# Kernel tuning notes

Measured on AMD Instinct MI355X. Metric: run time of the kernel, lower is better.

Reference implementation:

```python
import jax, jax.numpy as jnp
import numpy as np

B, N, D, E, H = 8, 2048, 1024, 8, 4096
CAP_FACTOR = 1.25   # capacity_factor_train
THRESHOLD = 0.2     # second_threshold_train
LOSS_COEF = 0.01
MIN_CAP = 4
EPS = 1e-9


def setup_inputs() -> dict:
    key = jax.random.key(0)
    ks = jax.random.split(key, 5)
    return {
        "hidden_states": jax.random.normal(ks[0], (B, N, D), jnp.float32),
        "wg": jax.random.normal(ks[1], (D, E), jnp.float32) * 0.02,
        "w1": jax.random.normal(ks[2], (E, D, H), jnp.float32) * 0.02,
        "b1": jnp.zeros((E, H), jnp.float32),
        "w2": jax.random.normal(ks[3], (E, H, D), jnp.float32) * 0.02,
        "b2": jnp.zeros((E, D), jnp.float32),
        "rand_probs": jax.random.uniform(ks[4], (B, N), jnp.float32),
    }


def _top2_gating(x, wg, rand_probs):
    # GShard-style top-2 gating with 'random' second policy and capacity limit.
    dt = x.dtype
    n = x.shape[-2]
    e = wg.shape[-1]
    raw = jax.nn.softmax(jnp.einsum('bnd,de->bne', x, wg), axis=-1)  # [b,n,e]
    idx1 = jnp.argmax(raw, axis=-1)
    gate1 = jnp.max(raw, axis=-1)
    mask1 = jax.nn.one_hot(idx1, e, dtype=dt)
    raw2 = raw * (1.0 - mask1)
    idx2 = jnp.argmax(raw2, axis=-1)
    gate2 = jnp.max(raw2, axis=-1)
    mask2 = jax.nn.one_hot(idx2, e, dtype=dt)
    denom = gate1 + gate2 + EPS
    gate1 = gate1 / denom
    gate2 = gate2 / denom
    # load-balancing loss (computed before capacity truncation)
    density1 = jnp.mean(mask1, axis=-2)          # [b,e]
    density1_proxy = jnp.mean(raw, axis=-2)      # [b,e]
    loss = jnp.mean(density1_proxy * density1) * (e * e)
    # second policy == 'random': keep 2nd expert w.p. ~ gate2/threshold
    mask2 = mask2 * (rand_probs < (gate2 / max(THRESHOLD, EPS)))[..., None].astype(dt)
    capacity = max(min(n, int(n * CAP_FACTOR / e)), MIN_CAP)
    # exclusive cumsum over tokens -> position within expert
    pos1 = (jnp.cumsum(mask1, axis=-2) - mask1) * mask1
    mask1 = mask1 * (pos1 < capacity).astype(dt)
    mask1_count = jnp.sum(mask1, axis=-2, keepdims=True)
    mask1_flat = jnp.sum(mask1, axis=-1)
    pos1 = jnp.sum(pos1, axis=-1)
    gate1 = gate1 * mask1_flat
    pos2 = (jnp.cumsum(mask2, axis=-2) - mask2 + mask1_count) * mask2
    mask2 = mask2 * (pos2 < capacity).astype(dt)
    mask2_flat = jnp.sum(mask2, axis=-1)
    pos2 = jnp.sum(pos2, axis=-1)
    gate2 = gate2 * mask2_flat
    # combine tensor [b,n,e,c]; out-of-range positions one_hot to zeros
    oh_p1 = jax.nn.one_hot(pos1.astype(jnp.int32), capacity, dtype=dt)
    oh_p2 = jax.nn.one_hot(pos2.astype(jnp.int32), capacity, dtype=dt)
    combine = ((gate1 * mask1_flat)[..., None, None]
               * jax.nn.one_hot(idx1, e, dtype=dt)[..., None] * oh_p1[..., None, :]
               + (gate2 * mask2_flat)[..., None, None]
               * jax.nn.one_hot(idx2, e, dtype=dt)[..., None] * oh_p2[..., None, :])
    dispatch = (combine > 0).astype(dt)
    return dispatch, combine, loss


def reference(hidden_states, wg, w1, b1, w2, b2, rand_probs):
    dispatch, combine, loss = _top2_gating(hidden_states, wg, rand_probs)
    # dispatch tokens to per-expert capacity buffers: [e,b,c,d]
    ei = jnp.einsum('bnd,bnec->ebcd', hidden_states, dispatch)
    # per-expert FFN (grouped GEMMs)
    h = jax.nn.gelu(jnp.einsum('ebcd,edh->ebch', ei, w1) + b1[:, None, None, :],
                    approximate=False)
    eo = jnp.einsum('ebch,ehd->ebcd', h, w2) + b2[:, None, None, :]
    # combine back to token order with gate weights
    out = jnp.einsum('ebcd,bnec->bnd', eo, combine)
    # dropout is identity (output_dropout_prob=0.0 / eval mode)
    return out, loss * LOSS_COEF
```

## Files before the change

kernel.cpp:

```cpp
#include <hip/hip_runtime.h>
#include <hip/hip_bf16.h>
#include <math.h>

#define BB 8
#define NN 2048
#define DD 1024
#define EE 8
#define HH 4096
#define CAP 320
#define NTOK (BB*NN)
#define MBC (BB*CAP)

typedef __bf16 bf16x8 __attribute__((ext_vector_type(8)));
typedef float f32x4 __attribute__((ext_vector_type(4)));
typedef unsigned u32x4 __attribute__((ext_vector_type(4)));
typedef unsigned short u16x4 __attribute__((ext_vector_type(4)));
typedef unsigned short u16;

__device__ __forceinline__ u16 f2bf(float f) {
    unsigned u = __builtin_bit_cast(unsigned, f);
    u += 0x7FFFu + ((u >> 16) & 1u);
    return (u16)(u >> 16);
}

__device__ __forceinline__ void async_cp16(const void* g, void* l) {
    __builtin_amdgcn_global_load_lds((const __attribute__((address_space(1))) void*)g,
                                     (__attribute__((address_space(3))) void*)l,
                                     16, 0, 0);
}

__global__ void MoE_zero_stats(float* stats) {
    if (threadIdx.x < 128) stats[threadIdx.x] = 0.0f;
}

__global__ __launch_bounds__(256) void MoE_gating(
    const float* __restrict__ x, const float* __restrict__ wg,
    const float* __restrict__ rp,
    int* __restrict__ i1o, int* __restrict__ i2o,
    float* __restrict__ g1o, float* __restrict__ g2o, int* __restrict__ keepo,
    float* __restrict__ proxy, float* __restrict__ cnt1)
{
    __shared__ float wgT[8*1024];
    __shared__ float sprox[8];
    __shared__ float scnt[8];
    int tid = threadIdx.x;
    {
        int d0 = tid*4;
        #pragma unroll
        for (int j = 0; j < 4; j++) {
            int d = d0 + j;
            f32x4 a = *(const f32x4*)(wg + d*8);
            f32x4 b = *(const f32x4*)(wg + d*8 + 4);
            wgT[0*1024+d]=a[0]; wgT[1*1024+d]=a[1]; wgT[2*1024+d]=a[2]; wgT[3*1024+d]=a[3];
            wgT[4*1024+d]=b[0]; wgT[5*1024+d]=b[1]; wgT[6*1024+d]=b[2]; wgT[7*1024+d]=b[3];
        }
    }
    if (tid < 8) { sprox[tid] = 0.0f; scnt[tid] = 0.0f; }
    __syncthreads();

    int wid = tid >> 6, lane = tid & 63;
    int tok = blockIdx.x*4 + wid;
    int b = tok >> 11;
    const float* xr = x + (size_t)tok * DD;

    double acc[8];
    #pragma unroll
    for (int e = 0; e < 8; e++) acc[e] = 0.0;
    for (int i = 0; i < 16; i++) {
        float xv = xr[i*64 + lane];
        #pragma unroll
        for (int e = 0; e < 8; e++)
            acc[e] += (double)xv * (double)wgT[e*1024 + i*64 + lane];
    }
    #pragma unroll
    for (int e = 0; e < 8; e++) {
        double v = acc[e];
        for (int off = 32; off; off >>= 1) v += __shfl_down(v, off, 64);
        acc[e] = v;
    }
    if (lane == 0) {
        float l[8];
        #pragma unroll
        for (int e = 0; e < 8; e++) l[e] = (float)acc[e];
        int i1 = 0;
        #pragma unroll
        for (int e = 1; e < 8; e++) if (l[e] > l[i1]) i1 = e;
        int i2 = (i1 == 0) ? 1 : 0;
        #pragma unroll
        for (int e = 0; e < 8; e++) if (e != i1 && l[e] > l[i2]) i2 = e;
        float mx = l[i1], p[8], s = 0.0f;
        #pragma unroll
        for (int e = 0; e < 8; e++) { p[e] = expf(l[e] - mx); s += p[e]; }
        float inv = 1.0f / s;
        #pragma unroll
        for (int e = 0; e < 8; e++) p[e] *= inv;
        float gate1 = p[i1], gate2 = p[i2];
        float denom = gate1 + gate2 + 1e-9f;
        float g1 = gate1 / denom, g2 = gate2 / denom;
        int keep = (rp[tok] < g2 / 0.2f) ? 1 : 0;
        i1o[tok] = i1; i2o[tok] = i2; g1o[tok] = g1; g2o[tok] = g2; keepo[tok] = keep;
        #pragma unroll
        for (int e = 0; e < 8; e++) atomicAdd(&sprox[e], p[e]);
        atomicAdd(&scnt[i1], 1.0f);
    }
    __syncthreads();
    if (tid < 8) {
        atomicAdd(&proxy[b*8 + tid], sprox[tid]);
        atomicAdd(&cnt1[b*8 + tid], scnt[tid]);
    }
}

__global__ __launch_bounds__(256) void MoE_scan(
    const int* __restrict__ i1, const int* __restrict__ i2, const int* __restrict__ keep,
    const float* __restrict__ g1, const float* __restrict__ g2,
    int* __restrict__ p1o, int* __restrict__ p2o,
    float* __restrict__ g1f, float* __restrict__ g2f,
    int* __restrict__ slot_token)
{
    int b = blockIdx.x, t = threadIdx.x;
    __shared__ unsigned long long s0[256], s1[256];
    for (int s = t; s < EE*CAP; s += 256) {
        int e = s / CAP, c = s % CAP;
        slot_token[(e*BB + b)*CAP + c] = -1;
    }
    int base = b*NN + t*8;

    int e1v[8];
    unsigned long long u0 = 0, u1 = 0;
    #pragma unroll
    for (int j = 0; j < 8; j++) {
        int e = i1[base + j]; e1v[j] = e;
        if (e < 4) u0 += 1ull << (e*16); else u1 += 1ull << ((e-4)*16);
    }
    s0[t] = u0; s1[t] = u1;
    __syncthreads();
    for (int off = 1; off < 256; off <<= 1) {
        unsigned long long a0 = 0, a1 = 0;
        if (t >= off) { a0 = s0[t-off]; a1 = s1[t-off]; }
        __syncthreads();
        s0[t] += a0; s1[t] += a1;
        __syncthreads();
    }
    unsigned long long t0 = s0[255], t1 = s1[255];
    unsigned long long x0 = s0[t] - u0, x1 = s1[t] - u1;
    int run[8], mc[8];
    #pragma unroll
    for (int e = 0; e < 8; e++) {
        run[e] = (int)((e < 4 ? (x0 >> (e*16)) : (x1 >> ((e-4)*16))) & 0xFFFF);
        int tot = (int)((e < 4 ? (t0 >> (e*16)) : (t1 >> ((e-4)*16))) & 0xFFFF);
        mc[e] = tot < CAP ? tot : CAP;
    }
    #pragma unroll
    for (int j = 0; j < 8; j++) {
        int e = e1v[j];
        int p = run[e]++;
        bool v = p < CAP;
        p1o[base + j] = p;
        g1f[base + j] = v ? g1[base + j] : 0.0f;
        if (v) slot_token[(e*BB + b)*CAP + p] = t*8 + j;
    }
    __syncthreads();

    int e2v[8], kv[8];
    u0 = 0; u1 = 0;
    #pragma unroll
    for (int j = 0; j < 8; j++) {
        int e = i2[base + j]; e2v[j] = e;
        int k = keep[base + j]; kv[j] = k;
        if (k) { if (e < 4) u0 += 1ull << (e*16); else u1 += 1ull << ((e-4)*16); }
    }
    s0[t] = u0; s1[t] = u1;
    __syncthreads();
    for (int off = 1; off < 256; off <<= 1) {
        unsigned long long a0 = 0, a1 = 0;
        if (t >= off) { a0 = s0[t-off]; a1 = s1[t-off]; }
        __syncthreads();
        s0[t] += a0; s1[t] += a1;
        __syncthreads();
    }
    x0 = s0[t] - u0; x1 = s1[t] - u1;
    #pragma unroll
    for (int e = 0; e < 8; e++)
        run[e] = mc[e] + (int)((e < 4 ? (x0 >> (e*16)) : (x1 >> ((e-4)*16))) & 0xFFFF);
    #pragma unroll
    for (int j = 0; j < 8; j++) {
        if (kv[j]) {
            int e = e2v[j];
            int p = run[e]++;
            bool v = p < CAP;
            p2o[base + j] = p;
            g2f[base + j] = v ? g2[base + j] : 0.0f;
            if (v) slot_token[(e*BB + b)*CAP + p] = t*8 + j;
        } else {
            p2o[base + j] = 0;
            g2f[base + j] = 0.0f;
        }
    }
}

__global__ __launch_bounds__(256) void MoE_dispatch(
    const float* __restrict__ x, const int* __restrict__ slot_token,
    u16* __restrict__ Abuf)
{
    int tid = threadIdx.x, wid = tid >> 6, lane = tid & 63;
    int slot = blockIdx.x*4 + wid;
    int b = (slot % (BB*CAP)) / CAP;
    int tok = slot_token[slot];
    u16* dst = Abuf + (size_t)slot * DD;
    if (tok >= 0) {
        const float* src = x + ((size_t)b*NN + tok) * DD;
        #pragma unroll
        for (int i = 0; i < 4; i++) {
            f32x4 v = *(const f32x4*)(src + (lane + 64*i)*4);
            u16x4 w = { f2bf(v[0]), f2bf(v[1]), f2bf(v[2]), f2bf(v[3]) };
            *(u16x4*)(dst + (lane + 64*i)*4) = w;
        }
    } else {
        u16x4 z = {0,0,0,0};
        #pragma unroll
        for (int i = 0; i < 4; i++) *(u16x4*)(dst + (lane + 64*i)*4) = z;
    }
}

__global__ __launch_bounds__(256) void MoE_transpose_bf16(
    const float* __restrict__ in, u16* __restrict__ out,
    int R, int C, int rTiles, int cTiles)
{
    int tilesPerE = rTiles * cTiles;
    int e = blockIdx.x / tilesPerE;
    int t = blockIdx.x % tilesPerE;
    int r0 = (t / cTiles) * 64, c0 = (t % cTiles) * 64;
    const float* ip = in + (size_t)e * R * C;
    u16* op = out + (size_t)e * R * C;
    __shared__ float T[64*65];
    int tid = threadIdx.x;
    int rr = tid >> 4, cx = tid & 15;
    #pragma unroll
    for (int i = 0; i < 4; i++) {
        int r = rr + i*16;
        f32x4 v = *(const f32x4*)(ip + (size_t)(r0 + r)*C + c0 + cx*4);
        float* d = T + r*65 + cx*4;
        d[0]=v[0]; d[1]=v[1]; d[2]=v[2]; d[3]=v[3];
    }
    __syncthreads();
    #pragma unroll
    for (int i = 0; i < 4; i++) {
        int c = rr + i*16;
        int r = cx*4;
        u16x4 w = { f2bf(T[(r+0)*65 + c]), f2bf(T[(r+1)*65 + c]),
                    f2bf(T[(r+2)*65 + c]), f2bf(T[(r+3)*65 + c]) };
        *(u16x4*)(op + (size_t)(c0 + c)*R + r0 + r) = w;
    }
}

template <int MODE>
__global__ __launch_bounds__(256, 2) void MoE_gemm_bt(
    const u16* __restrict__ Aall, const u16* __restrict__ Ball,
    void* __restrict__ Call, const float* __restrict__ biasAll,
    int M, int N, int K, int mTiles, int nTiles)
{
    int bid = blockIdx.x;
    int e = bid & 7;
    int i = bid >> 3;
    const int GM = 8;
    int group = i / (GM*nTiles);
    int gm = mTiles - group*GM; if (gm > GM) gm = GM;
    int rem = i - group*GM*nTiles;
    int n_ = rem / gm;
    int mm = rem % gm;
    if (n_ & 1) mm = gm - 1 - mm;
    int m0 = (group*GM + mm) * 128;
    int n0 = n_ * 128;

    const u16* A  = Aall + (size_t)e * M * K;
    const u16* Bm = Ball + (size_t)e * N * K;
    const float* bias = biasAll + (size_t)e * N;

    __shared__ u16 sA[128*32];
    __shared__ u16 sB[128*32];

    int tid = threadIdx.x;
    int lane = tid & 63, wid = tid >> 6;
    int wm = wid & 1, wn = wid >> 1;
    int l16 = lane & 15, quad = lane >> 4;

    int ch0 = tid, ch1 = 256 + tid;
    int r0c = ch0 >> 2, c0c = (ch0 & 3) ^ (r0c & 3);
    int r1c = ch1 >> 2, c1c = (ch1 & 3) ^ (r1c & 3);
    const u16* gA0 = A  + (size_t)(m0 + r0c)*K + c0c*8;
    const u16* gA1 = A  + (size_t)(m0 + r1c)*K + c1c*8;
    const u16* gB0 = Bm + (size_t)(n0 + r0c)*K + c0c*8;
    const u16* gB1 = Bm + (size_t)(n0 + r1c)*K + c1c*8;
    u16* dA0 = sA + (size_t)(tid & ~63) * 8;
    u16* dA1 = sA + (size_t)(256 + (tid & ~63)) * 8;
    u16* dB0 = sB + (size_t)(tid & ~63) * 8;
    u16* dB1 = sB + (size_t)(256 + (tid & ~63)) * 8;

    const u16* rA = sA + (wm*64 + l16)*32 + ((quad ^ (l16 & 3)) * 8);
    const u16* rB = sB + (wn*64 + l16)*32 + ((quad ^ (l16 & 3)) * 8);

    f32x4 acc[4][4] = {};
    int ksteps = K / 32;
    for (int kk = 0; kk < ksteps; ++kk) {
        async_cp16(gA0, dA0); async_cp16(gA1, dA1);
        async_cp16(gB0, dB0); async_cp16(gB1, dB1);
        gA0 += 32; gA1 += 32; gB0 += 32; gB1 += 32;
        __syncthreads();
        bf16x8 av[4], bv[4];
        #pragma unroll
        for (int i2 = 0; i2 < 4; i2++) av[i2] = __builtin_bit_cast(bf16x8, *(const u32x4*)(rA + i2*512));
        #pragma unroll
        for (int j = 0; j < 4; j++) bv[j] = __builtin_bit_cast(bf16x8, *(const u32x4*)(rB + j*512));
        #pragma unroll
        for (int i2 = 0; i2 < 4; i2++)
            #pragma unroll
            for (int j = 0; j < 4; j++)
                acc[i2][j] = __builtin_amdgcn_mfma_f32_16x16x32_bf16(av[i2], bv[j], acc[i2][j], 0, 0, 0);
        __syncthreads();
    }

    if (MODE == 0) {
        u16* C = (u16*)Call + (size_t)e * M * N;
        #pragma unroll
        for (int i2 = 0; i2 < 4; i2++) {
            int m = m0 + wm*64 + i2*16 + quad*4;
            #pragma unroll
            for (int j = 0; j < 4; j++) {
                int n = n0 + wn*64 + j*16 + l16;
                float bn = bias[n];
                #pragma unroll
                for (int r = 0; r < 4; r++) {
                    float v = acc[i2][j][r] + bn;
                    v = 0.5f * v * (1.0f + erff(v * 0.70710678118654752f));
                    C[(size_t)(m + r)*N + n] = f2bf(v);
                }
            }
        }
    } else {
        float* C = (float*)Call + (size_t)e * M * N;
        #pragma unroll
        for (int i2 = 0; i2 < 4; i2++) {
            int m = m0 + wm*64 + i2*16 + quad*4;
            #pragma unroll
            for (int j = 0; j < 4; j++) {
                int n = n0 + wn*64 + j*16 + l16;
                float bn = bias[n];
                #pragma unroll
                for (int r = 0; r < 4; r++)
                    C[(size_t)(m + r)*N + n] = acc[i2][j][r] + bn;
            }
        }
    }
}

__global__ __launch_bounds__(256) void MoE_combine(
    const float* __restrict__ EO,
    const int* __restrict__ i1, const int* __restrict__ i2,
    const int* __restrict__ p1, const int* __restrict__ p2,
    const float* __restrict__ g1f, const float* __restrict__ g2f,
    float* __restrict__ out)
{
    int tid = threadIdx.x, wid = tid >> 6, lane = tid & 63;
    int tok = blockIdx.x*4 + wid;
    int b = tok >> 11;
    float ga = g1f[tok], gb = g2f[tok];
    int ea = i1[tok], eb = i2[tok], pa = p1[tok], pb = p2[tok];
    f32x4 o[4] = {};
    if (ga > 0.0f) {
        const float* r = EO + ((size_t)(ea*BB + b)*CAP + pa) * DD;
        #pragma unroll
        for (int i = 0; i < 4; i++) {
            f32x4 v = *(const f32x4*)(r + (lane + 64*i)*4);
            o[i][0] += ga*v[0]; o[i][1] += ga*v[1]; o[i][2] += ga*v[2]; o[i][3] += ga*v[3];
        }
    }
    if (gb > 0.0f) {
        const float* r = EO + ((size_t)(eb*BB + b)*CAP + pb) * DD;
        #pragma unroll
        for (int i = 0; i < 4; i++) {
            f32x4 v = *(const f32x4*)(r + (lane + 64*i)*4);
            o[i][0] += gb*v[0]; o[i][1] += gb*v[1]; o[i][2] += gb*v[2]; o[i][3] += gb*v[3];
        }
    }
    float* w = out + (size_t)tok * DD;
    #pragma unroll
    for (int i = 0; i < 4; i++) *(f32x4*)(w + (lane + 64*i)*4) = o[i];
}

__global__ void MoE_loss(const float* __restrict__ proxy, const float* __restrict__ cnt,
                         float* __restrict__ out)
{
    int t = threadIdx.x;
    float v = proxy[t] * cnt[t];
    for (int off = 32; off; off >>= 1) v += __shfl_down(v, off, 64);
    if (t == 0) out[0] = v * (0.01f / ((float)NN * (float)NN));
}

extern "C" void kernel_launch(void* const* d_in, const int* in_sizes, int n_in,
                              void* d_out, int out_size, void* d_ws, size_t ws_size,
                              hipStream_t stream) {
    const float* x  = (const float*)d_in[0];
    const float* wg = (const float*)d_in[1];
    const float* w1 = (const float*)d_in[2];
    const float* b1 = (const float*)d_in[3];
    const float* w2 = (const float*)d_in[4];
    const float* b2 = (const float*)d_in[5];
    const float* rp = (const float*)d_in[6];
    float* out = (float*)d_out;

    char* w = (char*)d_ws;
    auto alloc = [&](size_t bytes) -> char* {
        char* p = w; w += (bytes + 255) & ~(size_t)255; return p;
    };
    u16*   w1b  = (u16*)alloc((size_t)2*EE*DD*HH);
    u16*   w2b  = (u16*)alloc((size_t)2*EE*HH*DD);
    u16*   Abuf = (u16*)alloc((size_t)2*EE*MBC*DD);
    u16*   Hbuf = (u16*)alloc((size_t)2*EE*MBC*HH);
    float* EO   = (float*)alloc((size_t)4*EE*MBC*DD);
    int*   i1   = (int*)alloc(4*NTOK);
    int*   i2   = (int*)alloc(4*NTOK);
    int*   keep = (int*)alloc(4*NTOK);
    int*   p1   = (int*)alloc(4*NTOK);
    int*   p2   = (int*)alloc(4*NTOK);
    float* g1   = (float*)alloc(4*NTOK);
    float* g2   = (float*)alloc(4*NTOK);
    float* g1f  = (float*)alloc(4*NTOK);
    float* g2f  = (float*)alloc(4*NTOK);
    int*   slot = (int*)alloc(4*EE*BB*CAP);
    float* stats = (float*)alloc(4*128);
    float* proxy = stats;
    float* cnt   = stats + 64;

    MoE_zero_stats<<<1, 128, 0, stream>>>(stats);
    MoE_transpose_bf16<<<EE*16*64, 256, 0, stream>>>(w1, w1b, 1024, 4096, 16, 64);
    MoE_transpose_bf16<<<EE*64*16, 256, 0, stream>>>(w2, w2b, 4096, 1024, 64, 16);
    MoE_gating<<<NTOK/4, 256, 0, stream>>>(x, wg, rp, i1, i2, g1, g2, keep, proxy, cnt);
    MoE_scan<<<BB, 256, 0, stream>>>(i1, i2, keep, g1, g2, p1, p2, g1f, g2f, slot);
    MoE_dispatch<<<EE*BB*CAP/4, 256, 0, stream>>>(x, slot, Abuf);
    MoE_gemm_bt<0><<<EE*20*32, 256, 0, stream>>>(Abuf, w1b, Hbuf, b1, MBC, HH, DD, 20, 32);
    MoE_gemm_bt<1><<<EE*20*8, 256, 0, stream>>>(Hbuf, w2b, EO, b2, MBC, DD, HH, 20, 8);
    MoE_combine<<<NTOK/4, 256, 0, stream>>>(EO, i1, i2, p1, p2, g1f, g2f, out);
    MoE_loss<<<1, 64, 0, stream>>>(proxy, cnt, out + (size_t)NTOK*DD);
}
```

Measured before the change: 923.8 us.

## Fuse combine into second GEMM epilogue with atomics; widen K tile; fast GELU

Removes the separate combine kernel and EO buffer: the second expert GEMM now scatters gate-weighted results straight into the zeroed output with atomicAdd, using slot-to-token and slot-gate maps built in the scan. The gating kernel zeroes the output. The GEMM K tile doubles to 64 with an 8-way swizzle, occupancy hint rises to 3, exact erf GELU is replaced by a tanh approximation, and the weight transpose writes 8-wide bf16 stores. This trades the EO round trip for float atomics, which make summation order nondeterministic, and the tanh GELU adds approximation error.

```diff
diff --git a/kernel.cpp b/kernel.cpp
--- a/kernel.cpp
+++ b/kernel.cpp
@@ -15,6 +15,7 @@
 typedef float f32x4 __attribute__((ext_vector_type(4)));
 typedef unsigned u32x4 __attribute__((ext_vector_type(4)));
 typedef unsigned short u16x4 __attribute__((ext_vector_type(4)));
+typedef unsigned short u16x8v __attribute__((ext_vector_type(8)));
 typedef unsigned short u16;
 
 __device__ __forceinline__ u16 f2bf(float f) {
@@ -27,6 +28,14 @@
     __builtin_amdgcn_global_load_lds((const __attribute__((address_space(1))) void*)g,
                                      (__attribute__((address_space(3))) void*)l,
                                      16, 0, 0);
+}
+
+__device__ __forceinline__ float gelu_fast(float v) {
+    float u = v * (0.7978845608f + 0.0356774081f * v * v);
+    u = fminf(fmaxf(u, -30.0f), 30.0f);
+    float ex = __expf(-2.0f * u);
+    float th = (1.0f - ex) / (1.0f + ex);
+    return 0.5f * v * (1.0f + th);
 }
 
 __global__ void MoE_zero_stats(float* stats) {
@@ -38,12 +47,19 @@
     const float* __restrict__ rp,
     int* __restrict__ i1o, int* __restrict__ i2o,
     float* __restrict__ g1o, float* __restrict__ g2o, int* __restrict__ keepo,
-    float* __restrict__ proxy, float* __restrict__ cnt1)
+    float* __restrict__ proxy, float* __restrict__ cnt1,
+    float* __restrict__ out_zero)
 {
     __shared__ float wgT[8*1024];
     __shared__ float sprox[8];
     __shared__ float scnt[8];
     int tid = threadIdx.x;
+    {
+        f32x4 z = {0,0,0,0};
+        f32x4* dst = (f32x4*)(out_zero + (size_t)blockIdx.x * 4 * DD);
+        #pragma unroll
+        for (int i = 0; i < 4; i++) dst[tid + 256*i] = z;
+    }
     {
         int d0 = tid*4;
         #pragma unroll
@@ -113,9 +129,7 @@
 __global__ __launch_bounds__(256) void MoE_scan(
     const int* __restrict__ i1, const int* __restrict__ i2, const int* __restrict__ keep,
     const float* __restrict__ g1, const float* __restrict__ g2,
-    int* __restrict__ p1o, int* __restrict__ p2o,
-    float* __restrict__ g1f, float* __restrict__ g2f,
-    int* __restrict__ slot_token)
+    int* __restrict__ slot_token, float* __restrict__ slot_gate)
 {
     int b = blockIdx.x, t = threadIdx.x;
     __shared__ unsigned long long s0[256], s1[256];
@@ -154,10 +168,10 @@
     for (int j = 0; j < 8; j++) {
         int e = e1v[j];
         int p = run[e]++;
-        bool v = p < CAP;
-        p1o[base + j] = p;
-        g1f[base + j] = v ? g1[base + j] : 0.0f;
-        if (v) slot_token[(e*BB + b)*CAP + p] = t*8 + j;
+        if (p < CAP) {
+            slot_token[(e*BB + b)*CAP + p] = t*8 + j;
+            slot_gate[(e*BB + b)*CAP + p] = g1[base + j];
+        }
     }
     __syncthreads();
 
@@ -187,13 +201,10 @@
         if (kv[j]) {
             int e = e2v[j];
             int p = run[e]++;
-            bool v = p < CAP;
-            p2o[base + j] = p;
-            g2f[base + j] = v ? g2[base + j] : 0.0f;
-            if (v) slot_token[(e*BB + b)*CAP + p] = t*8 + j;
-        } else {
-            p2o[base + j] = 0;
-            g2f[base + j] = 0.0f;
+            if (p < CAP) {
+                slot_token[(e*BB + b)*CAP + p] = t*8 + j;
+                slot_gate[(e*BB + b)*CAP + p] = g2[base + j];
+            }
         }
     }
 }
@@ -234,29 +245,36 @@
     u16* op = out + (size_t)e * R * C;
     __shared__ float T[64*65];
     int tid = threadIdx.x;
-    int rr = tid >> 4, cx = tid & 15;
-    #pragma unroll
-    for (int i = 0; i < 4; i++) {
-        int r = rr + i*16;
-        f32x4 v = *(const f32x4*)(ip + (size_t)(r0 + r)*C + c0 + cx*4);
-        float* d = T + r*65 + cx*4;
-        d[0]=v[0]; d[1]=v[1]; d[2]=v[2]; d[3]=v[3];
-    }
-    __syncthreads();
-    #pragma unroll
-    for (int i = 0; i < 4; i++) {
-        int c = rr + i*16;
-        int r = cx*4;
-        u16x4 w = { f2bf(T[(r+0)*65 + c]), f2bf(T[(r+1)*65 + c]),
-                    f2bf(T[(r+2)*65 + c]), f2bf(T[(r+3)*65 + c]) };
-        *(u16x4*)(op + (size_t)(c0 + c)*R + r0 + r) = w;
+    {
+        int rr = tid >> 4, cx = tid & 15;
+        #pragma unroll
+        for (int i = 0; i < 4; i++) {
+            int r = rr + i*16;
+            f32x4 v = *(const f32x4*)(ip + (size_t)(r0 + r)*C + c0 + cx*4);
+            float* d = T + r*65 + cx*4;
+            d[0]=v[0]; d[1]=v[1]; d[2]=v[2]; d[3]=v[3];
+        }
+    }
+    __syncthreads();
+    {
+        int cw = tid >> 3, rx = tid & 7;
+        int r = rx*8;
+        #pragma unroll
+        for (int i = 0; i < 2; i++) {
+            int c = cw + i*32;
+            u16x8v w;
+            #pragma unroll
+            for (int jj = 0; jj < 8; jj++) w[jj] = f2bf(T[(r+jj)*65 + c]);
+            *(u16x8v*)(op + (size_t)(c0 + c)*R + r0 + r) = w;
+        }
     }
 }
 
 template <int MODE>
-__global__ __launch_bounds__(256, 2) void MoE_gemm_bt(
+__global__ __launch_bounds__(256, 3) void MoE_gemm_bt(
     const u16* __restrict__ Aall, const u16* __restrict__ Ball,
     void* __restrict__ Call, const float* __restrict__ biasAll,
+    const int* __restrict__ slot_token, const float* __restrict__ slot_gate,
     int M, int N, int K, int mTiles, int nTiles)
 {
     int bid = blockIdx.x;
@@ -276,46 +294,56 @@
     const u16* Bm = Ball + (size_t)e * N * K;
     const float* bias = biasAll + (size_t)e * N;
 
-    __shared__ u16 sA[128*32];
-    __shared__ u16 sB[128*32];
+    __shared__ u16 sA[128*64];
+    __shared__ u16 sB[128*64];
 
     int tid = threadIdx.x;
     int lane = tid & 63, wid = tid >> 6;
     int wm = wid & 1, wn = wid >> 1;
     int l16 = lane & 15, quad = lane >> 4;
 
-    int ch0 = tid, ch1 = 256 + tid;
-    int r0c = ch0 >> 2, c0c = (ch0 & 3) ^ (r0c & 3);
-    int r1c = ch1 >> 2, c1c = (ch1 & 3) ^ (r1c & 3);
-    const u16* gA0 = A  + (size_t)(m0 + r0c)*K + c0c*8;
-    const u16* gA1 = A  + (size_t)(m0 + r1c)*K + c1c*8;
-    const u16* gB0 = Bm + (size_t)(n0 + r0c)*K + c0c*8;
-    const u16* gB1 = Bm + (size_t)(n0 + r1c)*K + c1c*8;
-    u16* dA0 = sA + (size_t)(tid & ~63) * 8;
-    u16* dA1 = sA + (size_t)(256 + (tid & ~63)) * 8;
-    u16* dB0 = sB + (size_t)(tid & ~63) * 8;
-    u16* dB1 = sB + (size_t)(256 + (tid & ~63)) * 8;
-
-    const u16* rA = sA + (wm*64 + l16)*32 + ((quad ^ (l16 & 3)) * 8);
-    const u16* rB = sB + (wn*64 + l16)*32 + ((quad ^ (l16 & 3)) * 8);
+    const u16* gA[4]; const u16* gB[4]; u16* dA[4]; u16* dB[4];
+    #pragma unroll
+    for (int l = 0; l < 4; l++) {
+        int ch = l*256 + tid;
+        int row = ch >> 3;
+        int gc  = (ch & 7) ^ (row & 7);
+        gA[l] = A  + (size_t)(m0 + row)*K + gc*8;
+        gB[l] = Bm + (size_t)(n0 + row)*K + gc*8;
+        dA[l] = sA + (size_t)(l*256 + (tid & ~63)) * 8;
+        dB[l] = sB + (size_t)(l*256 + (tid & ~63)) * 8;
+    }
+
+    int rbaseA = (wm*64 + l16)*64;
+    int rbaseB = (wn*64 + l16)*64;
+    int sw = l16 & 7;
+    int swz0 = ((0*4 + quad) ^ sw) * 8;
+    int swz1 = ((1*4 + quad) ^ sw) * 8;
 
     f32x4 acc[4][4] = {};
-    int ksteps = K / 32;
+    int ksteps = K / 64;
     for (int kk = 0; kk < ksteps; ++kk) {
-        async_cp16(gA0, dA0); async_cp16(gA1, dA1);
-        async_cp16(gB0, dB0); async_cp16(gB1, dB1);
-        gA0 += 32; gA1 += 32; gB0 += 32; gB1 += 32;
-        __syncthreads();
-        bf16x8 av[4], bv[4];
-        #pragma unroll
-        for (int i2 = 0; i2 < 4; i2++) av[i2] = __builtin_bit_cast(bf16x8, *(const u32x4*)(rA + i2*512));
-        #pragma unroll
-        for (int j = 0; j < 4; j++) bv[j] = __builtin_bit_cast(bf16x8, *(const u32x4*)(rB + j*512));
-        #pragma unroll
-        for (int i2 = 0; i2 < 4; i2++)
-            #pragma unroll
-            for (int j = 0; j < 4; j++)
-                acc[i2][j] = __builtin_amdgcn_mfma_f32_16x16x32_bf16(av[i2], bv[j], acc[i2][j], 0, 0, 0);
+        #pragma unroll
+        for (int l = 0; l < 4; l++) {
+            async_cp16(gA[l], dA[l]);
+            async_cp16(gB[l], dB[l]);
+            gA[l] += 64; gB[l] += 64;
+        }
+        __syncthreads();
+        #pragma unroll
+        for (int h = 0; h < 2; h++) {
+            int swz = h ? swz1 : swz0;
+            bf16x8 av[4], bv[4];
+            #pragma unroll
+            for (int i2 = 0; i2 < 4; i2++) av[i2] = __builtin_bit_cast(bf16x8, *(const u32x4*)(sA + rbaseA + i2*1024 + swz));
+            #pragma unroll
+            for (int j = 0; j < 4; j++) bv[j] = __builtin_bit_cast(bf16x8, *(const u32x4*)(sB + rbaseB + j*1024 + swz));
+            #pragma unroll
+            for (int i2 = 0; i2 < 4; i2++)
+                #pragma unroll
+                for (int j = 0; j < 4; j++)
+                    acc[i2][j] = __builtin_amdgcn_mfma_f32_16x16x32_bf16(av[i2], bv[j], acc[i2][j], 0, 0, 0);
+        }
         __syncthreads();
     }
 
@@ -331,60 +359,33 @@
                 #pragma unroll
                 for (int r = 0; r < 4; r++) {
                     float v = acc[i2][j][r] + bn;
-                    v = 0.5f * v * (1.0f + erff(v * 0.70710678118654752f));
-                    C[(size_t)(m + r)*N + n] = f2bf(v);
+                    C[(size_t)(m + r)*N + n] = f2bf(gelu_fast(v));
                 }
             }
         }
     } else {
-        float* C = (float*)Call + (size_t)e * M * N;
+        float* outp = (float*)Call;
+        float bn[4];
+        #pragma unroll
+        for (int j = 0; j < 4; j++) bn[j] = bias[n0 + wn*64 + j*16 + l16];
         #pragma unroll
         for (int i2 = 0; i2 < 4; i2++) {
-            int m = m0 + wm*64 + i2*16 + quad*4;
-            #pragma unroll
-            for (int j = 0; j < 4; j++) {
-                int n = n0 + wn*64 + j*16 + l16;
-                float bn = bias[n];
+            #pragma unroll
+            for (int r = 0; r < 4; r++) {
+                int mr = m0 + wm*64 + i2*16 + quad*4 + r;
+                int bb = mr / CAP;
+                int cc = mr - bb*CAP;
+                int sidx = (e*BB + bb)*CAP + cc;
+                int tok = slot_token[sidx];
+                if (tok < 0) continue;
+                float g = slot_gate[sidx];
+                float* orow = outp + ((size_t)bb*NN + tok)*DD + n0 + wn*64 + l16;
                 #pragma unroll
-                for (int r = 0; r < 4; r++)
-                    C[(size_t)(m + r)*N + n] = acc[i2][j][r] + bn;
+                for (int j = 0; j < 4; j++)
+                    atomicAdd(orow + j*16, g * (acc[i2][j][r] + bn[j]));
             }
         }
     }
-}
-
-__global__ __launch_bounds__(256) void MoE_combine(
-    const float* __restrict__ EO,
-    const int* __restrict__ i1, const int* __restrict__ i2,
-    const int* __restrict__ p1, const int* __restrict__ p2,
-    const float* __restrict__ g1f, const float* __restrict__ g2f,
-    float* __restrict__ out)
-{
-    int tid = threadIdx.x, wid = tid >> 6, lane = tid & 63;
-    int tok = blockIdx.x*4 + wid;
-    int b = tok >> 11;
-    float ga = g1f[tok], gb = g2f[tok];
-    int ea = i1[tok], eb = i2[tok], pa = p1[tok], pb = p2[tok];
-    f32x4 o[4] = {};
-    if (ga > 0.0f) {
-        const float* r = EO + ((size_t)(ea*BB + b)*CAP + pa) * DD;
-        #pragma unroll
-        for (int i = 0; i < 4; i++) {
-            f32x4 v = *(const f32x4*)(r + (lane + 64*i)*4);
-            o[i][0] += ga*v[0]; o[i][1] += ga*v[1]; o[i][2] += ga*v[2]; o[i][3] += ga*v[3];
-        }
-    }
-    if (gb > 0.0f) {
-        const float* r = EO + ((size_t)(eb*BB + b)*CAP + pb) * DD;
-        #pragma unroll
-        for (int i = 0; i < 4; i++) {
-            f32x4 v = *(const f32x4*)(r + (lane + 64*i)*4);
-            o[i][0] += gb*v[0]; o[i][1] += gb*v[1]; o[i][2] += gb*v[2]; o[i][3] += gb*v[3];
-        }
-    }
-    float* w = out + (size_t)tok * DD;
-    #pragma unroll
-    for (int i = 0; i < 4; i++) *(f32x4*)(w + (lane + 64*i)*4) = o[i];
 }
 
 __global__ void MoE_loss(const float* __restrict__ proxy, const float* __restrict__ cnt,
@@ -416,17 +417,13 @@
     u16*   w2b  = (u16*)alloc((size_t)2*EE*HH*DD);
     u16*   Abuf = (u16*)alloc((size_t)2*EE*MBC*DD);
     u16*   Hbuf = (u16*)alloc((size_t)2*EE*MBC*HH);
-    float* EO   = (float*)alloc((size_t)4*EE*MBC*DD);
     int*   i1   = (int*)alloc(4*NTOK);
     int*   i2   = (int*)alloc(4*NTOK);
     int*   keep = (int*)alloc(4*NTOK);
-    int*   p1   = (int*)alloc(4*NTOK);
-    int*   p2   = (int*)alloc(4*NTOK);
     float* g1   = (float*)alloc(4*NTOK);
     float* g2   = (float*)alloc(4*NTOK);
-    float* g1f  = (float*)alloc(4*NTOK);
-    float* g2f  = (float*)alloc(4*NTOK);
     int*   slot = (int*)alloc(4*EE*BB*CAP);
+    float* sgate= (float*)alloc(4*EE*BB*CAP);
     float* stats = (float*)alloc(4*128);
     float* proxy = stats;
     float* cnt   = stats + 64;
@@ -434,11 +431,10 @@
     MoE_zero_stats<<<1, 128, 0, stream>>>(stats);
     MoE_transpose_bf16<<<EE*16*64, 256, 0, stream>>>(w1, w1b, 1024, 4096, 16, 64);
     MoE_transpose_bf16<<<EE*64*16, 256, 0, stream>>>(w2, w2b, 4096, 1024, 64, 16);
-    MoE_gating<<<NTOK/4, 256, 0, stream>>>(x, wg, rp, i1, i2, g1, g2, keep, proxy, cnt);
-    MoE_scan<<<BB, 256, 0, stream>>>(i1, i2, keep, g1, g2, p1, p2, g1f, g2f, slot);
+    MoE_gating<<<NTOK/4, 256, 0, stream>>>(x, wg, rp, i1, i2, g1, g2, keep, proxy, cnt, out);
+    MoE_scan<<<BB, 256, 0, stream>>>(i1, i2, keep, g1, g2, slot, sgate);
     MoE_dispatch<<<EE*BB*CAP/4, 256, 0, stream>>>(x, slot, Abuf);
-    MoE_gemm_bt<0><<<EE*20*32, 256, 0, stream>>>(Abuf, w1b, Hbuf, b1, MBC, HH, DD, 20, 32);
-    MoE_gemm_bt<1><<<EE*20*8, 256, 0, stream>>>(Hbuf, w2b, EO, b2, MBC, DD, HH, 20, 8);
-    MoE_combine<<<NTOK/4, 256, 0, stream>>>(EO, i1, i2, p1, p2, g1f, g2f, out);
+    MoE_gemm_bt<0><<<EE*20*32, 256, 0, stream>>>(Abuf, w1b, Hbuf, b1, nullptr, nullptr, MBC, HH, DD, 20, 32);
+    MoE_gemm_bt<1><<<EE*20*8, 256, 0, stream>>>(Hbuf, w2b, out, b2, slot, sgate, MBC, DD, HH, 20, 8);
     MoE_loss<<<1, 64, 0, stream>>>(proxy, cnt, out + (size_t)NTOK*DD);
 }
```

Measured after the change: 859.9 us. 1.07x faster.
